# Optimization experiments

Hardware: AMD Instinct MI355X
Metric: run time of the kernel (lower is better)

## Reference

```python
import jax, jax.numpy as jnp
import numpy as np

N_COM = 100  # number of communities


def _gat(x, src, dst, ew, W, a_s, a_d):
    # Weighted multi-head GAT layer. x: [N,F], src/dst: [E], ew: [E]
    N = x.shape[0]
    H, dh = a_s.shape
    h = (x @ W).reshape(N, H, dh)              # [N,H,dh]
    hs, hd = h[src], h[dst]                     # [E,H,dh]
    e = jax.nn.leaky_relu((hs * a_s).sum(-1) + (hd * a_d).sum(-1), 0.2)  # [E,H]
    m = jax.ops.segment_max(e, dst, num_segments=N)  # [N,H] stable softmax max
    m = jnp.where(jnp.isfinite(m), m, 0.0)
    ex = jnp.exp(e - m[dst]) * ew[:, None]      # edge-weighted attention numerator
    den = jax.ops.segment_sum(ex, dst, num_segments=N)          # [N,H]
    num = jax.ops.segment_sum(ex[:, :, None] * hs, dst, num_segments=N)  # [N,H,dh]
    out = num / (den[:, :, None] + 1e-16)
    return jax.nn.elu(out.reshape(N, H * dh))


def _meso(x, part, D):
    # WeiPool_noW: degree-weighted mean pooling per community, scattered back to nodes
    num = jax.ops.segment_sum(D[:, None] * x, part, num_segments=N_COM)  # [C,d]
    den = jax.ops.segment_sum(D, part, num_segments=N_COM)               # [C]
    mean = num / (den[:, None] + 1e-16)
    return mean[part]                                                     # [N,d]


def _lstm_cell(h, c, x, Wx, Wh, b):
    z = x @ Wx + h @ Wh + b
    i, f, g, o = jnp.split(z, 4, axis=-1)
    c = jax.nn.sigmoid(f) * c + jax.nn.sigmoid(i) * jnp.tanh(g)
    h = jax.nn.sigmoid(o) * jnp.tanh(c)
    return h, c


def setup_inputs() -> dict:
    key = jax.random.key(0)
    ks = jax.random.split(key, 20)
    T, N, E, F = 8, 10000, 320000, 128
    H = 4
    d1, d2 = 128, 64            # micro_dims[1], micro_dims[2]
    d_rnn = 128                 # RNN_dims[1]; RNN input = 2*d2 = 128
    d_dec = 64                  # decoder_dims[1]
    s = 0.05
    inp = {
        'feat': jax.random.normal(ks[0], (T, N, F), jnp.float32),
        'edge_weight': jax.random.uniform(ks[1], (T, E), jnp.float32),
        'D': jax.random.uniform(ks[2], (T, N), jnp.float32),
        'W1': jax.random.normal(ks[3], (F, d1), jnp.float32) * s,
        'a_src1': jax.random.normal(ks[4], (H, d1 // H), jnp.float32) * s,
        'a_dst1': jax.random.normal(ks[5], (H, d1 // H), jnp.float32) * s,
        'W2': jax.random.normal(ks[6], (d1, d2), jnp.float32) * s,
        'a_src2': jax.random.normal(ks[7], (H, d2 // H), jnp.float32) * s,
        'a_dst2': jax.random.normal(ks[8], (H, d2 // H), jnp.float32) * s,
        'Wx': jax.random.normal(ks[9], (2 * d2, 4 * d_rnn), jnp.float32) * s,
        'Wh': jax.random.normal(ks[10], (d_rnn, 4 * d_rnn), jnp.float32) * s,
        'b_lstm': jnp.zeros((4 * d_rnn,), jnp.float32),
        'emb_W': jax.random.normal(ks[11], (d_rnn, d_dec), jnp.float32) * s,
        'emb_b': jnp.zeros((d_dec,), jnp.float32),
        'scal_W': jax.random.normal(ks[12], (d_rnn, d_dec), jnp.float32) * s,
        'scal_b': jnp.zeros((d_dec,), jnp.float32),
        'edge_index': jax.random.randint(ks[13], (T, 2, E), 0, N, jnp.int64),
        'partition': jax.random.randint(ks[14], (T, N), 0, N_COM, jnp.int64),
    }
    return inp


def reference(feat, edge_weight, D, W1, a_src1, a_dst1, W2, a_src2, a_dst2,
              Wx, Wh, b_lstm, emb_W, emb_b, scal_W, scal_b,
              edge_index, partition):
    T, N, _ = feat.shape
    src, dst = edge_index[:, 0], edge_index[:, 1]          # [T,E]
    gat = jax.vmap(_gat, in_axes=(0, 0, 0, 0, None, None, None))
    g1 = gat(feat, src, dst, edge_weight, W1, a_src1, a_dst1)   # [T,N,d1]
    g2 = gat(g1, src, dst, edge_weight, W2, a_src2, a_dst2)     # [T,N,d2]
    meso = jax.vmap(_meso)(g2, partition, D)                    # [T,N,d2]
    agg = jnp.concatenate([g2, meso], axis=-1)                  # [T,N,2*d2]

    d_h = Wh.shape[0]
    h0 = jnp.zeros((N, d_h), feat.dtype)

    def step(carry, x):
        h, c = carry
        h, c = _lstm_cell(h, c, x, Wx, Wh, b_lstm)
        return (h, c), h

    _, hs = jax.lax.scan(step, (h0, h0), agg)                   # [T,N,d_h]
    h_last = hs[-1]

    emb = jnp.tanh(h_last @ emb_W + emb_b)                      # decoder emb path
    emb = emb / jnp.linalg.norm(emb, axis=0, keepdims=True)     # F.normalize dim=0
    scal = jax.nn.sigmoid(h_last @ scal_W + scal_b)             # decoder scal path
    S = scal @ scal.T                                            # [N,N]
    G = emb @ emb.T
    sq = jnp.diag(G)
    dist = -(sq[:, None] + sq[None, :] - 2.0 * G)                # -||e_i - e_j||^2
    adj_est = 1.0 + jnp.tanh(dist * S)
    return adj_est
```

## Files before the change

kernel.cpp:

```cpp
#include <hip/hip_runtime.h>
#include <cstddef>
#include <cstdint>

#define T_   8
#define N_   10000
#define E_   320000
#define F_   128
#define D1_  128
#define D2_  64
#define DR_  128
#define NC_  100
#define TN_  (T_*N_)
#define TE_  (T_*E_)
#define NPAD_ 10112

typedef __attribute__((ext_vector_type(8))) short bf16x8;
typedef __attribute__((ext_vector_type(8))) ushort u16x8;
typedef __attribute__((ext_vector_type(4))) float f32x4;

__device__ __forceinline__ float bf2f(ushort u) {
    return __uint_as_float(((unsigned int)u) << 16);
}
__device__ __forceinline__ ushort f2bf(float f) {
    unsigned int u = __float_as_uint(f);
    unsigned int r = (u + 0x7FFFu + ((u >> 16) & 1u)) >> 16;
    return (ushort)r;
}
__device__ __forceinline__ float fast_tanh(float x) {
    float t = __expf(2.f * x);
    return 1.f - 2.f / (t + 1.f);
}
__device__ __forceinline__ float fast_sigmoid(float x) {
    return 1.f / (1.f + __expf(-x));
}

__global__ __launch_bounds__(256) void conv_feat(const float* __restrict__ src,
                                                 ushort* __restrict__ dst, int n8)
{
    int idx = blockIdx.x * 256 + threadIdx.x;
    if (idx >= n8) return;
    const float4* s = (const float4*)src + (size_t)idx * 2;
    float4 x = s[0], y = s[1];
    u16x8 o;
    o[0]=f2bf(x.x); o[1]=f2bf(x.y); o[2]=f2bf(x.z); o[3]=f2bf(x.w);
    o[4]=f2bf(y.x); o[5]=f2bf(y.y); o[6]=f2bf(y.z); o[7]=f2bf(y.w);
    *((u16x8*)dst + idx) = o;
}

__global__ __launch_bounds__(256) void conv_weights(
    const float* __restrict__ W1, const float* __restrict__ W2,
    const float* __restrict__ Wx, const float* __restrict__ Wh,
    const float* __restrict__ eW, const float* __restrict__ sW,
    ushort* __restrict__ W1T, ushort* __restrict__ W2T,
    ushort* __restrict__ WxT, ushort* __restrict__ WhT,
    ushort* __restrict__ eWT, ushort* __restrict__ sWT)
{
    int idx = blockIdx.x * 256 + threadIdx.x;
    if (idx < 16384)       { int n=idx>>7,   k=idx&127;            W1T[idx]=f2bf(W1[k*128+n]); }
    else if (idx < 24576)  { int l=idx-16384;  int n=l>>7,k=l&127; W2T[l]=f2bf(W2[k*64+n]); }
    else if (idx < 90112)  { int l=idx-24576;  int n=l>>7,k=l&127; WxT[l]=f2bf(Wx[k*512+n]); }
    else if (idx < 155648) { int l=idx-90112;  int n=l>>7,k=l&127; WhT[l]=f2bf(Wh[k*512+n]); }
    else if (idx < 163840) { int l=idx-155648; int n=l>>7,k=l&127; eWT[l]=f2bf(eW[k*64+n]); }
    else if (idx < 172032) { int l=idx-163840; int n=l>>7,k=l&127; sWT[l]=f2bf(sW[k*64+n]); }
}

__global__ __launch_bounds__(256) void gemm_bf16(
    const ushort* __restrict__ A, const ushort* __restrict__ BT,
    float* __restrict__ Cf, ushort* __restrict__ Cb,
    const float* __restrict__ bias, const float* __restrict__ addsrc,
    int M, int K, int Nc, int act)
{
    int w = threadIdx.x >> 6, lane = threadIdx.x & 63;
    int quad = lane >> 4, l16 = lane & 15;
    int m0 = blockIdx.y * 128 + w * 32;
    int n0 = blockIdx.x * 64;
    f32x4 zf = {0.f, 0.f, 0.f, 0.f};
    f32x4 acc[2][4];
    #pragma unroll
    for (int rt = 0; rt < 2; ++rt)
        #pragma unroll
        for (int ct = 0; ct < 4; ++ct) acc[rt][ct] = zf;

    for (int k0 = 0; k0 < K; k0 += 32) {
        int kk = k0 + quad * 8;
        bf16x8 a0 = *(const bf16x8*)(A + (size_t)(m0 + l16) * K + kk);
        bf16x8 a1 = *(const bf16x8*)(A + (size_t)(m0 + 16 + l16) * K + kk);
        bf16x8 b[4];
        #pragma unroll
        for (int ct = 0; ct < 4; ++ct)
            b[ct] = *(const bf16x8*)(BT + (size_t)(n0 + ct * 16 + l16) * K + kk);
        #pragma unroll
        for (int ct = 0; ct < 4; ++ct) {
            acc[0][ct] = __builtin_amdgcn_mfma_f32_16x16x32_bf16(a0, b[ct], acc[0][ct], 0, 0, 0);
            acc[1][ct] = __builtin_amdgcn_mfma_f32_16x16x32_bf16(a1, b[ct], acc[1][ct], 0, 0, 0);
        }
    }

    #pragma unroll
    for (int rt = 0; rt < 2; ++rt) {
        int ibase = m0 + rt * 16 + quad * 4;
        #pragma unroll
        for (int r = 0; r < 4; ++r) {
            int i = ibase + r;
            if (i >= M) continue;
            #pragma unroll
            for (int ct = 0; ct < 4; ++ct) {
                int j = n0 + ct * 16 + l16;
                float v = acc[rt][ct][r];
                if (bias)   v += bias[j];
                if (addsrc) v += addsrc[(size_t)i * Nc + j];
                if (act == 1)      v = fast_tanh(v);
                else if (act == 2) v = fast_sigmoid(v);
                if (Cf) Cf[(size_t)i * Nc + j] = v;
                if (Cb) Cb[(size_t)i * Nc + j] = f2bf(v);
            }
        }
    }
}

__global__ __launch_bounds__(256) void att_vec128(
    const ushort* __restrict__ h, const float* __restrict__ a_src,
    const float* __restrict__ a_dst, float* __restrict__ as_out,
    float* __restrict__ ad_out, int rows)
{
    int wid  = (blockIdx.x * 256 + threadIdx.x) >> 6;
    int lane = threadIdx.x & 63;
    if (wid >= rows) return;
    const ushort* hr = h + (size_t)wid * 128;
    float v0 = bf2f(hr[lane]), v1 = bf2f(hr[64 + lane]);
    float pa0 = v0 * a_src[lane], pa1 = v1 * a_src[64 + lane];
    float pd0 = v0 * a_dst[lane], pd1 = v1 * a_dst[64 + lane];
    #pragma unroll
    for (int m = 1; m <= 16; m <<= 1) {
        pa0 += __shfl_xor(pa0, m); pa1 += __shfl_xor(pa1, m);
        pd0 += __shfl_xor(pd0, m); pd1 += __shfl_xor(pd1, m);
    }
    if ((lane & 31) == 0) {
        int g = lane >> 5;
        as_out[wid * 4 + g] = pa0; as_out[wid * 4 + 2 + g] = pa1;
        ad_out[wid * 4 + g] = pd0; ad_out[wid * 4 + 2 + g] = pd1;
    }
}

__global__ __launch_bounds__(256) void att_vec64(
    const ushort* __restrict__ h, const float* __restrict__ a_src,
    const float* __restrict__ a_dst, float* __restrict__ as_out,
    float* __restrict__ ad_out, int rows)
{
    int wid  = (blockIdx.x * 256 + threadIdx.x) >> 6;
    int lane = threadIdx.x & 63;
    if (wid >= rows) return;
    float v = bf2f(h[(size_t)wid * 64 + lane]);
    float pa = v * a_src[lane], pd = v * a_dst[lane];
    #pragma unroll
    for (int m = 1; m <= 8; m <<= 1) { pa += __shfl_xor(pa, m); pd += __shfl_xor(pd, m); }
    if ((lane & 15) == 0) {
        int g = lane >> 4;
        as_out[wid * 4 + g] = pa; ad_out[wid * 4 + g] = pd;
    }
}

__global__ void count_edges(const int* __restrict__ eidx, int* __restrict__ counts)
{
    int idx = blockIdx.x * 256 + threadIdx.x;
    if (idx >= TE_) return;
    int t = idx / E_, e = idx - t * E_;
    int d = eidx[(size_t)t * 2 * E_ + E_ + e];
    atomicAdd(&counts[t * N_ + d], 1);
}

__global__ __launch_bounds__(1024) void scan_per_t(
    const int* __restrict__ counts, int* __restrict__ rowptr, int* __restrict__ cursor)
{
    const int CH = 10;
    int t = blockIdx.x, i = threadIdx.x;
    int base0 = t * N_;
    int cnt[CH];
    int s = 0;
    int g0 = i * CH;
    #pragma unroll
    for (int q = 0; q < CH; ++q) {
        int g = g0 + q;
        cnt[q] = (g < N_) ? counts[base0 + g] : 0;
        s += cnt[q];
    }
    __shared__ int buf[1024];
    buf[i] = s;
    __syncthreads();
    for (int off = 1; off < 1024; off <<= 1) {
        int v = (i >= off) ? buf[i - off] : 0;
        __syncthreads();
        buf[i] += v;
        __syncthreads();
    }
    int run = t * E_ + buf[i] - s;
    #pragma unroll
    for (int q = 0; q < CH; ++q) {
        int g = g0 + q;
        if (g < N_) {
            rowptr[base0 + g] = run;
            cursor[base0 + g] = run;
            run += cnt[q];
        }
    }
    if (t == T_ - 1 && i == 1023) rowptr[T_ * N_] = TE_;
}

__global__ void fill_csr(const int* __restrict__ eidx, const float* __restrict__ ew,
                         int* __restrict__ cursor, int* __restrict__ src_csr,
                         float* __restrict__ ew_csr)
{
    int idx = blockIdx.x * 256 + threadIdx.x;
    if (idx >= TE_) return;
    int t = idx / E_, e = idx - t * E_;
    int s = eidx[(size_t)t * 2 * E_ + e];
    int d = eidx[(size_t)t * 2 * E_ + E_ + e];
    float w = ew[(size_t)t * E_ + e];
    int pos = atomicAdd(&cursor[t * N_ + d], 1);
    src_csr[pos] = t * N_ + s;
    ew_csr[pos] = w;
}

__global__ __launch_bounds__(256) void gat_node_128(
    const ushort* __restrict__ h, const float* __restrict__ as,
    const float* __restrict__ ad, const int* __restrict__ rowptr,
    const int* __restrict__ src_csr, const float* __restrict__ ew_csr,
    ushort* __restrict__ outp, int rows)
{
    int wid  = (blockIdx.x * 256 + threadIdx.x) >> 6;
    int lane = threadIdx.x & 63;
    if (wid >= rows) return;
    int start = rowptr[wid], end = rowptr[wid + 1];
    int h0 = lane >> 5;
    float ad0 = ad[wid * 4 + h0], ad1 = ad[wid * 4 + 2 + h0];
    float acc0 = 0.f, acc1 = 0.f, den0 = 0.f, den1 = 0.f;

    int p = start;
    for (; p + 4 <= end; p += 4) {
        int s0 = src_csr[p+0], s1 = src_csr[p+1], s2 = src_csr[p+2], s3 = src_csr[p+3];
        float w0 = ew_csr[p+0], w1 = ew_csr[p+1], w2 = ew_csr[p+2], w3 = ew_csr[p+3];
        float4 A0 = *(const float4*)(as + (size_t)s0 * 4);
        float4 A1 = *(const float4*)(as + (size_t)s1 * 4);
        float4 A2 = *(const float4*)(as + (size_t)s2 * 4);
        float4 A3 = *(const float4*)(as + (size_t)s3 * 4);
        const ushort* q0 = h + (size_t)s0 * 128;
        const ushort* q1 = h + (size_t)s1 * 128;
        const ushort* q2 = h + (size_t)s2 * 128;
        const ushort* q3 = h + (size_t)s3 * 128;
        float hx0 = bf2f(q0[lane]), hy0 = bf2f(q0[64 + lane]);
        float hx1 = bf2f(q1[lane]), hy1 = bf2f(q1[64 + lane]);
        float hx2 = bf2f(q2[lane]), hy2 = bf2f(q2[64 + lane]);
        float hx3 = bf2f(q3[lane]), hy3 = bf2f(q3[64 + lane]);
        #define GSTEP(AA, ww, hx, hy) { \
            float e0 = (h0 ? AA.y : AA.x) + ad0; e0 = e0 > 0.f ? e0 : 0.2f * e0; \
            float e1 = (h0 ? AA.w : AA.z) + ad1; e1 = e1 > 0.f ? e1 : 0.2f * e1; \
            float x0 = __expf(e0) * ww, x1 = __expf(e1) * ww; \
            den0 += x0; den1 += x1; acc0 += x0 * hx; acc1 += x1 * hy; }
        GSTEP(A0, w0, hx0, hy0)
        GSTEP(A1, w1, hx1, hy1)
        GSTEP(A2, w2, hx2, hy2)
        GSTEP(A3, w3, hx3, hy3)
    }
    for (; p < end; ++p) {
        int s = src_csr[p];
        float w = ew_csr[p];
        float4 A = *(const float4*)(as + (size_t)s * 4);
        const ushort* q = h + (size_t)s * 128;
        float hx = bf2f(q[lane]), hy = bf2f(q[64 + lane]);
        GSTEP(A, w, hx, hy)
    }
    #undef GSTEP

    float o0 = acc0 / (den0 + 1e-16f);
    float o1 = acc1 / (den1 + 1e-16f);
    o0 = o0 > 0.f ? o0 : (__expf(o0) - 1.f);
    o1 = o1 > 0.f ? o1 : (__expf(o1) - 1.f);
    outp[(size_t)wid * 128 + lane]      = f2bf(o0);
    outp[(size_t)wid * 128 + 64 + lane] = f2bf(o1);
}

__global__ __launch_bounds__(256) void gat_node_64(
    const ushort* __restrict__ h, const float* __restrict__ as,
    const float* __restrict__ ad, const int* __restrict__ rowptr,
    const int* __restrict__ src_csr, const float* __restrict__ ew_csr,
    ushort* __restrict__ outp, int rows)
{
    int wid  = (blockIdx.x * 256 + threadIdx.x) >> 6;
    int lane = threadIdx.x & 63;
    if (wid >= rows) return;
    int start = rowptr[wid], end = rowptr[wid + 1];
    int hh = lane >> 4;
    float adv = ad[wid * 4 + hh];
    float acc = 0.f, den = 0.f;

    int p = start;
    for (; p + 4 <= end; p += 4) {
        int s0 = src_csr[p+0], s1 = src_csr[p+1], s2 = src_csr[p+2], s3 = src_csr[p+3];
        float w0 = ew_csr[p+0], w1 = ew_csr[p+1], w2 = ew_csr[p+2], w3 = ew_csr[p+3];
        float4 A0 = *(const float4*)(as + (size_t)s0 * 4);
        float4 A1 = *(const float4*)(as + (size_t)s1 * 4);
        float4 A2 = *(const float4*)(as + (size_t)s2 * 4);
        float4 A3 = *(const float4*)(as + (size_t)s3 * 4);
        float hv0 = bf2f(h[(size_t)s0 * 64 + lane]);
        float hv1 = bf2f(h[(size_t)s1 * 64 + lane]);
        float hv2 = bf2f(h[(size_t)s2 * 64 + lane]);
        float hv3 = bf2f(h[(size_t)s3 * 64 + lane]);
        #define GSTEP64(AA, ww, hv) { \
            float e = (hh & 2 ? (hh & 1 ? AA.w : AA.z) : (hh & 1 ? AA.y : AA.x)) + adv; \
            e = e > 0.f ? e : 0.2f * e; \
            float x = __expf(e) * ww; \
            den += x; acc += x * hv; }
        GSTEP64(A0, w0, hv0)
        GSTEP64(A1, w1, hv1)
        GSTEP64(A2, w2, hv2)
        GSTEP64(A3, w3, hv3)
    }
    for (; p < end; ++p) {
        int s = src_csr[p];
        float w = ew_csr[p];
        float4 A = *(const float4*)(as + (size_t)s * 4);
        float hv = bf2f(h[(size_t)s * 64 + lane]);
        GSTEP64(A, w, hv)
    }
    #undef GSTEP64

    float o = acc / (den + 1e-16f);
    o = o > 0.f ? o : (__expf(o) - 1.f);
    outp[(size_t)wid * 64 + lane] = f2bf(o);
}

__global__ __launch_bounds__(256) void meso_acc(
    const ushort* __restrict__ g2, const int* __restrict__ part,
    const float* __restrict__ Dw, float* __restrict__ msum, float* __restrict__ mden)
{
    int wid  = (blockIdx.x * 256 + threadIdx.x) >> 6;
    int lane = threadIdx.x & 63;
    if (wid >= TN_) return;
    int t = wid / N_;
    int p = part[wid];
    float dv = Dw[wid];
    atomicAdd(&msum[((size_t)(t * NC_ + p) << 6) + lane], dv * bf2f(g2[(size_t)wid * 64 + lane]));
    if (lane == 0) atomicAdd(&mden[t * NC_ + p], dv);
}

__global__ void agg_assemble(
    const ushort* __restrict__ g2, const int* __restrict__ part,
    const float* __restrict__ msum, const float* __restrict__ mden,
    ushort* __restrict__ agg)
{
    int idx = blockIdx.x * 256 + threadIdx.x;
    int row = idx >> 7, d = idx & 127;
    ushort v;
    if (d < 64) {
        v = g2[(size_t)row * 64 + d];
    } else {
        int t = row / N_;
        int p = part[row];
        v = f2bf(msum[((size_t)(t * NC_ + p) << 6) + (d - 64)] / (mden[t * NC_ + p] + 1e-16f));
    }
    agg[idx] = v;
}

__global__ __launch_bounds__(512) void lstm_fused(
    const ushort* __restrict__ hin, const ushort* __restrict__ WhT,
    const float* __restrict__ zx, float* __restrict__ c,
    ushort* __restrict__ hout)
{
    __shared__ float zt[32][516];
    int w = threadIdx.x >> 6, lane = threadIdx.x & 63;
    int quad = lane >> 4, l16 = lane & 15;
    int m0 = blockIdx.x * 32;
    int n0 = w * 64;

    f32x4 zf = {0.f, 0.f, 0.f, 0.f};
    f32x4 acc[2][4];
    #pragma unroll
    for (int rt = 0; rt < 2; ++rt)
        #pragma unroll
        for (int ct = 0; ct < 4; ++ct) acc[rt][ct] = zf;

    #pragma unroll
    for (int k0 = 0; k0 < 128; k0 += 32) {
        int kk = k0 + quad * 8;
        bf16x8 a0 = *(const bf16x8*)(hin + (size_t)(m0 + l16) * 128 + kk);
        bf16x8 a1 = *(const bf16x8*)(hin + (size_t)(m0 + 16 + l16) * 128 + kk);
        bf16x8 b[4];
        #pragma unroll
        for (int ct = 0; ct < 4; ++ct)
            b[ct] = *(const bf16x8*)(WhT + (size_t)(n0 + ct * 16 + l16) * 128 + kk);
        #pragma unroll
        for (int ct = 0; ct < 4; ++ct) {
            acc[0][ct] = __builtin_amdgcn_mfma_f32_16x16x32_bf16(a0, b[ct], acc[0][ct], 0, 0, 0);
            acc[1][ct] = __builtin_amdgcn_mfma_f32_16x16x32_bf16(a1, b[ct], acc[1][ct], 0, 0, 0);
        }
    }

    #pragma unroll
    for (int rt = 0; rt < 2; ++rt) {
        #pragma unroll
        for (int r = 0; r < 4; ++r) {
            int li = rt * 16 + quad * 4 + r;
            size_t gi = (size_t)(m0 + li);
            #pragma unroll
            for (int ct = 0; ct < 4; ++ct) {
                int j = n0 + ct * 16 + l16;
                zt[li][j] = acc[rt][ct][r] + zx[gi * 512 + j];
            }
        }
    }
    __syncthreads();

    int r  = threadIdx.x >> 4;
    int j0 = (threadIdx.x & 15) * 8;
    int gi = m0 + r;
    if (gi < N_) {
        f32x4 vi[2], vf[2], vg[2], vo[2], vc[2];
        #pragma unroll
        for (int hb = 0; hb < 2; ++hb) {
            int jj = j0 + hb * 4;
            vi[hb] = *(const f32x4*)&zt[r][jj];
            vf[hb] = *(const f32x4*)&zt[r][128 + jj];
            vg[hb] = *(const f32x4*)&zt[r][256 + jj];
            vo[hb] = *(const f32x4*)&zt[r][384 + jj];
            vc[hb] = *(const f32x4*)(c + (size_t)gi * 128 + jj);
        }
        u16x8 ho;
        #pragma unroll
        for (int e = 0; e < 8; ++e) {
            int hb = e >> 2, q = e & 3;
            float si = fast_sigmoid(vi[hb][q]);
            float sf = fast_sigmoid(vf[hb][q]);
            float so = fast_sigmoid(vo[hb][q]);
            float cn = sf * vc[hb][q] + si * fast_tanh(vg[hb][q]);
            vc[hb][q] = cn;
            ho[e] = f2bf(so * fast_tanh(cn));
        }
        *(f32x4*)(c + (size_t)gi * 128 + j0)     = vc[0];
        *(f32x4*)(c + (size_t)gi * 128 + j0 + 4) = vc[1];
        *(u16x8*)(hout + (size_t)gi * 128 + j0)  = ho;
    }
}

__global__ __launch_bounds__(256) void col_sumsq(const float* __restrict__ emb,
                                                 float* __restrict__ colss)
{
    int tid = threadIdx.x;
    int col = tid & 63, rq = tid >> 6;
    float s = 0.f;
    for (int r = blockIdx.x * 4 + rq; r < N_; r += 40 * 4) {
        float v = emb[(size_t)r * 64 + col];
        s += v * v;
    }
    __shared__ float red[256];
    red[tid] = s;
    __syncthreads();
    if (tid < 64)
        atomicAdd(&colss[tid], red[tid] + red[tid + 64] + red[tid + 128] + red[tid + 192]);
}

__global__ __launch_bounds__(256) void norm_rows(const float* __restrict__ emb,
                                                 const float* __restrict__ colss,
                                                 ushort* __restrict__ embb,
                                                 float* __restrict__ sq, int rows)
{
    int wid  = (blockIdx.x * 256 + threadIdx.x) >> 6;
    int lane = threadIdx.x & 63;
    if (wid >= rows) return;
    float nv = emb[(size_t)wid * 64 + lane] / sqrtf(colss[lane]);
    ushort ub = f2bf(nv);
    embb[(size_t)wid * 64 + lane] = ub;
    float nq = bf2f(ub);
    float q = nq * nq;
    #pragma unroll
    for (int m = 1; m <= 32; m <<= 1) q += __shfl_xor(q, m);
    if (lane == 0) sq[wid] = q;
}

#define FTJ_   5
#define FCOLS_ (FTJ_*128)

__global__ __launch_bounds__(256) void final_adj_mfma(
    const ushort* __restrict__ embb, const ushort* __restrict__ scalb,
    const float* __restrict__ sq, float* __restrict__ outp)
{
    __shared__ float cur[128][132];
    __shared__ float edg[2][64][16];

    int w = threadIdx.x >> 6, lane = threadIdx.x & 63;
    int quad = lane >> 4, l16 = lane & 15;
    int bi = blockIdx.y * 128;
    int Wb = blockIdx.x * FCOLS_;
    int wi = bi + (w >> 1) * 64;

    float sqi[4];
    #pragma unroll
    for (int rt = 0; rt < 4; ++rt) sqi[rt] = sq[wi + rt * 16 + l16];

    int tLast = (N_ - 1 - Wb) / 128;
    if (tLast > FTJ_ - 1) tLast = FTJ_ - 1;

    for (int t = 0; t <= tLast; ++t) {
        int Wt = Wb + t * 128;
        int wj = Wt + (w & 1) * 64;

        f32x4 zf = {0.f, 0.f, 0.f, 0.f};
        f32x4 accG[4][4], accS[4][4];
        #pragma unroll
        for (int rt = 0; rt < 4; ++rt)
            #pragma unroll
            for (int ct = 0; ct < 4; ++ct) { accG[rt][ct] = zf; accS[rt][ct] = zf; }

        #pragma unroll
        for (int ks = 0; ks < 2; ++ks) {
            int k0 = ks * 32 + quad * 8;
            bf16x8 ae[4], af[4], be[4], bs[4];
            #pragma unroll
            for (int q = 0; q < 4; ++q) {
                int ri = wi + q * 16 + l16;
                int rj = wj + q * 16 + l16;
                ae[q] = *(const bf16x8*)(embb  + (size_t)ri * 64 + k0);
                af[q] = *(const bf16x8*)(scalb + (size_t)ri * 64 + k0);
                be[q] = *(const bf16x8*)(embb  + (size_t)rj * 64 + k0);
                bs[q] = *(const bf16x8*)(scalb + (size_t)rj * 64 + k0);
            }
            #pragma unroll
            for (int rt = 0; rt < 4; ++rt)
                #pragma unroll
                for (int ct = 0; ct < 4; ++ct) {
                    accG[rt][ct] = __builtin_amdgcn_mfma_f32_16x16x32_bf16(be[ct], ae[rt], accG[rt][ct], 0, 0, 0);
                    accS[rt][ct] = __builtin_amdgcn_mfma_f32_16x16x32_bf16(bs[ct], af[rt], accS[rt][ct], 0, 0, 0);
                }
        }

        __syncthreads();

        #pragma unroll
        for (int rt = 0; rt < 4; ++rt) {
            int li = (w >> 1) * 64 + rt * 16 + l16;
            float si = sqi[rt];
            #pragma unroll
            for (int ct = 0; ct < 4; ++ct) {
                int lj = (w & 1) * 64 + ct * 16 + quad * 4;
                const float4 sj = *(const float4*)(sq + Wt + lj);
                float sjr[4] = { sj.x, sj.y, sj.z, sj.w };
                f32x4 v;
                #pragma unroll
                for (int r = 0; r < 4; ++r) {
                    float G = accG[rt][ct][r], S = accS[rt][ct][r];
                    float dist = 2.f * G - si - sjr[r];
                    float e = __expf(2.f * dist * S);
                    v[r] = 2.f - 2.f / (e + 1.f);
                }
                *(f32x4*)&cur[li][lj] = v;
                if ((w & 1) && ct == 3 && (li & 1))
                    *(f32x4*)&edg[t & 1][li >> 1][quad * 4] = v;
            }
        }

        __syncthreads();

        int lane5 = lane & 31;
        #pragma unroll
        for (int pass = 0; pass < 16; ++pass) {
            int r = pass * 8 + (lane >> 5) * 4 + w;
            int i = bi + r;
            if (i < N_) {
                if (!(r & 1)) {
                    int gcol = Wt + lane5 * 4;
                    if (gcol < N_)
                        __builtin_nontemporal_store(*(const f32x4*)&cur[r][lane5 * 4],
                            (f32x4*)(outp + (size_t)i * N_ + gcol));
                } else {
                    int gcol = Wt - 16 + lane5 * 4;
                    if ((t > 0 || lane5 >= 4) && gcol >= 0 && gcol < N_) {
                        f32x4 v;
                        if (lane5 < 4) v = *(const f32x4*)&edg[(t & 1) ^ 1][r >> 1][lane5 * 4];
                        else           v = *(const f32x4*)&cur[r][lane5 * 4 - 16];
                        __builtin_nontemporal_store(v,
                            (f32x4*)(outp + (size_t)i * N_ + gcol));
                    }
                }
            }
        }
    }

    {
        int tid = threadIdx.x;
        int r = ((tid >> 2) << 1) | 1;
        int k = (tid & 3) * 4;
        int i = bi + r;
        int gcol = Wb + tLast * 128 + 112 + k;
        if (i < N_ && gcol < N_) {
            f32x4 v = *(const f32x4*)&cur[r][112 + k];
            __builtin_nontemporal_store(v, (f32x4*)(outp + (size_t)i * N_ + gcol));
        }
    }
}

extern "C" void kernel_launch(void* const* d_in, const int* in_sizes, int n_in,
                              void* d_out, int out_size, void* d_ws, size_t ws_size,
                              hipStream_t stream)
{
    (void)in_sizes; (void)n_in; (void)out_size; (void)ws_size;
    const float* feat    = (const float*)d_in[0];
    const float* eweight = (const float*)d_in[1];
    const float* Dw      = (const float*)d_in[2];
    const float* W1      = (const float*)d_in[3];
    const float* a_src1  = (const float*)d_in[4];
    const float* a_dst1  = (const float*)d_in[5];
    const float* W2      = (const float*)d_in[6];
    const float* a_src2  = (const float*)d_in[7];
    const float* a_dst2  = (const float*)d_in[8];
    const float* Wx      = (const float*)d_in[9];
    const float* Wh      = (const float*)d_in[10];
    const float* b_lstm  = (const float*)d_in[11];
    const float* emb_W   = (const float*)d_in[12];
    const float* emb_b   = (const float*)d_in[13];
    const float* scal_W  = (const float*)d_in[14];
    const float* scal_b  = (const float*)d_in[15];
    const int*   eidx    = (const int*)d_in[16];
    const int*   part    = (const int*)d_in[17];

    float* out = (float*)d_out;
    ushort* h1b   = (ushort*)(out + 0);
    ushort* g1b   = (ushort*)(out + 5120000);
    ushort* h2b   = (ushort*)(out + 10240000);
    ushort* g2b   = (ushort*)(out + 12800000);
    float* as1    = out + 15360000;
    float* ad1    = out + 15680000;
    float* as2    = out + 16000000;
    float* ad2    = out + 16320000;
    int*   rowptr = (int*)(out + 16640000);
    int*   cursor = (int*)(out + 16720064);
    int*   counts = (int*)(out + 16800064);
    int*   src_csr= (int*)(out + 16880064);
    float* ew_csr = out + 19440064;
    float* msum   = out + 22000064;
    float* mden   = out + 22051264;
    ushort* aggb  = (ushort*)(out + 22052064);
    float* ZX     = out + 27172064;
    float* cstate = out + 73252064;
    ushort* hbf   = (ushort*)(out + 74532064);
    ushort* featb = (ushort*)(out + 75179232);
    ushort* W1T   = (ushort*)(out + 80299232);
    ushort* W2T   = (ushort*)(out + 80307424);
    ushort* WxT   = (ushort*)(out + 80311520);
    ushort* WhT   = (ushort*)(out + 80344288);
    ushort* eWT   = (ushort*)(out + 80377056);
    ushort* sWT   = (ushort*)(out + 80381152);
    float* embf   = out + 80385248;
    float* colss  = out + 81025248;

    ushort* embb  = (ushort*)d_ws;
    ushort* scalb = embb + (size_t)NPAD_ * 64;
    float*  sq    = (float*)(scalb + (size_t)NPAD_ * 64);

    hipMemsetAsync(counts, 0, TN_ * sizeof(int), stream);
    hipMemsetAsync(msum, 0, (T_ * NC_ * 64 + T_ * NC_) * sizeof(float), stream);
    hipMemsetAsync(cstate, 0, (size_t)N_ * DR_ * sizeof(float), stream);
    hipMemsetAsync(hbf, 0, (size_t)NPAD_ * DR_ * sizeof(ushort), stream);
    hipMemsetAsync(colss, 0, 64 * sizeof(float), stream);

    conv_feat<<<5000, 256, 0, stream>>>(feat, featb, TN_ * F_ / 8);
    conv_weights<<<672, 256, 0, stream>>>(W1, W2, Wx, Wh, emb_W, scal_W,
                                          W1T, W2T, WxT, WhT, eWT, sWT);

    gemm_bf16<<<dim3(2, 625), 256, 0, stream>>>(featb, W1T, nullptr, h1b, nullptr, nullptr, TN_, 128, 128, 0);
    att_vec128<<<TN_/4, 256, 0, stream>>>(h1b, a_src1, a_dst1, as1, ad1, TN_);
    count_edges<<<(TE_+255)/256, 256, 0, stream>>>(eidx, counts);
    scan_per_t<<<T_, 1024, 0, stream>>>(counts, rowptr, cursor);
    fill_csr<<<(TE_+255)/256, 256, 0, stream>>>(eidx, eweight, cursor, src_csr, ew_csr);
    gat_node_128<<<TN_/4, 256, 0, stream>>>(h1b, as1, ad1, rowptr, src_csr, ew_csr, g1b, TN_);

    gemm_bf16<<<dim3(1, 625), 256, 0, stream>>>(g1b, W2T, nullptr, h2b, nullptr, nullptr, TN_, 128, 64, 0);
    att_vec64<<<TN_/4, 256, 0, stream>>>(h2b, a_src2, a_dst2, as2, ad2, TN_);
    gat_node_64<<<TN_/4, 256, 0, stream>>>(h2b, as2, ad2, rowptr, src_csr, ew_csr, g2b, TN_);

    meso_acc<<<TN_/4, 256, 0, stream>>>(g2b, part, Dw, msum, mden);
    agg_assemble<<<TN_*128/256, 256, 0, stream>>>(g2b, part, msum, mden, aggb);

    gemm_bf16<<<dim3(8, 625), 256, 0, stream>>>(aggb, WxT, ZX, nullptr, b_lstm, nullptr, TN_, 128, 512, 0);
    for (int t = 0; t < T_; ++t)
        lstm_fused<<<(N_ + 31) / 32, 512, 0, stream>>>(hbf, WhT, ZX + (size_t)t * N_ * 512,
                                                       cstate, hbf);

    gemm_bf16<<<dim3(1, 79), 256, 0, stream>>>(hbf, eWT, embf, nullptr, emb_b, nullptr, N_, 128, 64, 1);
    gemm_bf16<<<dim3(1, 79), 256, 0, stream>>>(hbf, sWT, nullptr, scalb, scal_b, nullptr, N_, 128, 64, 2);
    col_sumsq<<<40, 256, 0, stream>>>(embf, colss);
    norm_rows<<<(N_+3)/4, 256, 0, stream>>>(embf, colss, embb, sq, N_);

    final_adj_mfma<<<dim3(16, 79), 256, 0, stream>>>(embb, scalb, sq, out);
}
```

Before: 1.640 ms.

## Interleave CSR src/weight, widen GAT edge unroll, privatize meso pooling in LDS

Stores each CSR edge as an interleaved int2 (source index, weight bits) so the GAT aggregation kernels fetch both with one 16-byte vector load per two edges. The inner loop unrolls to 8 edges after an alignment peel, putting more independent gathers in flight. Meso pooling switches from per-node global atomics to per-block LDS histograms per timestep that are flushed once with global atomics, cutting global atomic contention. The cost is more register pressure from the wider unroll and only 128 blocks for the meso kernel.

```diff
diff --git a/kernel.cpp b/kernel.cpp
--- a/kernel.cpp
+++ b/kernel.cpp
@@ -207,8 +207,7 @@
 }
 
 __global__ void fill_csr(const int* __restrict__ eidx, const float* __restrict__ ew,
-                         int* __restrict__ cursor, int* __restrict__ src_csr,
-                         float* __restrict__ ew_csr)
+                         int* __restrict__ cursor, int2* __restrict__ csr)
 {
     int idx = blockIdx.x * 256 + threadIdx.x;
     if (idx >= TE_) return;
@@ -217,15 +216,13 @@
     int d = eidx[(size_t)t * 2 * E_ + E_ + e];
     float w = ew[(size_t)t * E_ + e];
     int pos = atomicAdd(&cursor[t * N_ + d], 1);
-    src_csr[pos] = t * N_ + s;
-    ew_csr[pos] = w;
+    csr[pos] = make_int2(t * N_ + s, __float_as_int(w));
 }
 
 __global__ __launch_bounds__(256) void gat_node_128(
     const ushort* __restrict__ h, const float* __restrict__ as,
     const float* __restrict__ ad, const int* __restrict__ rowptr,
-    const int* __restrict__ src_csr, const float* __restrict__ ew_csr,
-    ushort* __restrict__ outp, int rows)
+    const int2* __restrict__ csr, ushort* __restrict__ outp, int rows)
 {
     int wid  = (blockIdx.x * 256 + threadIdx.x) >> 6;
     int lane = threadIdx.x & 63;
@@ -235,38 +232,50 @@
     float ad0 = ad[wid * 4 + h0], ad1 = ad[wid * 4 + 2 + h0];
     float acc0 = 0.f, acc1 = 0.f, den0 = 0.f, den1 = 0.f;
 
+    #define GSTEP(AA, ww, hx, hy) { \
+        float e0 = (h0 ? AA.y : AA.x) + ad0; e0 = e0 > 0.f ? e0 : 0.2f * e0; \
+        float e1 = (h0 ? AA.w : AA.z) + ad1; e1 = e1 > 0.f ? e1 : 0.2f * e1; \
+        float x0 = __expf(e0) * ww, x1 = __expf(e1) * ww; \
+        den0 += x0; den1 += x1; acc0 += x0 * hx; acc1 += x1 * hy; }
+
     int p = start;
-    for (; p + 4 <= end; p += 4) {
-        int s0 = src_csr[p+0], s1 = src_csr[p+1], s2 = src_csr[p+2], s3 = src_csr[p+3];
-        float w0 = ew_csr[p+0], w1 = ew_csr[p+1], w2 = ew_csr[p+2], w3 = ew_csr[p+3];
-        float4 A0 = *(const float4*)(as + (size_t)s0 * 4);
-        float4 A1 = *(const float4*)(as + (size_t)s1 * 4);
-        float4 A2 = *(const float4*)(as + (size_t)s2 * 4);
-        float4 A3 = *(const float4*)(as + (size_t)s3 * 4);
-        const ushort* q0 = h + (size_t)s0 * 128;
-        const ushort* q1 = h + (size_t)s1 * 128;
-        const ushort* q2 = h + (size_t)s2 * 128;
-        const ushort* q3 = h + (size_t)s3 * 128;
-        float hx0 = bf2f(q0[lane]), hy0 = bf2f(q0[64 + lane]);
-        float hx1 = bf2f(q1[lane]), hy1 = bf2f(q1[64 + lane]);
-        float hx2 = bf2f(q2[lane]), hy2 = bf2f(q2[64 + lane]);
-        float hx3 = bf2f(q3[lane]), hy3 = bf2f(q3[64 + lane]);
-        #define GSTEP(AA, ww, hx, hy) { \
-            float e0 = (h0 ? AA.y : AA.x) + ad0; e0 = e0 > 0.f ? e0 : 0.2f * e0; \
-            float e1 = (h0 ? AA.w : AA.z) + ad1; e1 = e1 > 0.f ? e1 : 0.2f * e1; \
-            float x0 = __expf(e0) * ww, x1 = __expf(e1) * ww; \
-            den0 += x0; den1 += x1; acc0 += x0 * hx; acc1 += x1 * hy; }
-        GSTEP(A0, w0, hx0, hy0)
-        GSTEP(A1, w1, hx1, hy1)
-        GSTEP(A2, w2, hx2, hy2)
-        GSTEP(A3, w3, hx3, hy3)
+    if ((p & 1) && p < end) {
+        int2 E = csr[p];
+        float4 A = *(const float4*)(as + (size_t)E.x * 4);
+        const ushort* q = h + (size_t)E.x * 128;
+        float hx = bf2f(q[lane]), hy = bf2f(q[64 + lane]);
+        float w = __int_as_float(E.y);
+        GSTEP(A, w, hx, hy)
+        ++p;
+    }
+    for (; p + 8 <= end; p += 8) {
+        int4 e0 = *(const int4*)(csr + p);
+        int4 e1 = *(const int4*)(csr + p + 2);
+        int4 e2 = *(const int4*)(csr + p + 4);
+        int4 e3 = *(const int4*)(csr + p + 6);
+        int ss[8] = { e0.x, e0.z, e1.x, e1.z, e2.x, e2.z, e3.x, e3.z };
+        float wwv[8] = { __int_as_float(e0.y), __int_as_float(e0.w),
+                         __int_as_float(e1.y), __int_as_float(e1.w),
+                         __int_as_float(e2.y), __int_as_float(e2.w),
+                         __int_as_float(e3.y), __int_as_float(e3.w) };
+        float4 Av[8];
+        #pragma unroll
+        for (int q = 0; q < 8; ++q) Av[q] = *(const float4*)(as + (size_t)ss[q] * 4);
+        float hx[8], hy[8];
+        #pragma unroll
+        for (int q = 0; q < 8; ++q) {
+            const ushort* hp = h + (size_t)ss[q] * 128;
+            hx[q] = bf2f(hp[lane]); hy[q] = bf2f(hp[64 + lane]);
+        }
+        #pragma unroll
+        for (int q = 0; q < 8; ++q) GSTEP(Av[q], wwv[q], hx[q], hy[q])
     }
     for (; p < end; ++p) {
-        int s = src_csr[p];
-        float w = ew_csr[p];
-        float4 A = *(const float4*)(as + (size_t)s * 4);
-        const ushort* q = h + (size_t)s * 128;
+        int2 E = csr[p];
+        float4 A = *(const float4*)(as + (size_t)E.x * 4);
+        const ushort* q = h + (size_t)E.x * 128;
         float hx = bf2f(q[lane]), hy = bf2f(q[64 + lane]);
+        float w = __int_as_float(E.y);
         GSTEP(A, w, hx, hy)
     }
     #undef GSTEP
@@ -282,8 +291,7 @@
 __global__ __launch_bounds__(256) void gat_node_64(
     const ushort* __restrict__ h, const float* __restrict__ as,
     const float* __restrict__ ad, const int* __restrict__ rowptr,
-    const int* __restrict__ src_csr, const float* __restrict__ ew_csr,
-    ushort* __restrict__ outp, int rows)
+    const int2* __restrict__ csr, ushort* __restrict__ outp, int rows)
 {
     int wid  = (blockIdx.x * 256 + threadIdx.x) >> 6;
     int lane = threadIdx.x & 63;
@@ -293,33 +301,45 @@
     float adv = ad[wid * 4 + hh];
     float acc = 0.f, den = 0.f;
 
+    #define GSTEP64(AA, ww, hv) { \
+        float e = (hh & 2 ? (hh & 1 ? AA.w : AA.z) : (hh & 1 ? AA.y : AA.x)) + adv; \
+        e = e > 0.f ? e : 0.2f * e; \
+        float x = __expf(e) * ww; \
+        den += x; acc += x * hv; }
+
     int p = start;
-    for (; p + 4 <= end; p += 4) {
-        int s0 = src_csr[p+0], s1 = src_csr[p+1], s2 = src_csr[p+2], s3 = src_csr[p+3];
-        float w0 = ew_csr[p+0], w1 = ew_csr[p+1], w2 = ew_csr[p+2], w3 = ew_csr[p+3];
-        float4 A0 = *(const float4*)(as + (size_t)s0 * 4);
-        float4 A1 = *(const float4*)(as + (size_t)s1 * 4);
-        float4 A2 = *(const float4*)(as + (size_t)s2 * 4);
-        float4 A3 = *(const float4*)(as + (size_t)s3 * 4);
-        float hv0 = bf2f(h[(size_t)s0 * 64 + lane]);
-        float hv1 = bf2f(h[(size_t)s1 * 64 + lane]);
-        float hv2 = bf2f(h[(size_t)s2 * 64 + lane]);
-        float hv3 = bf2f(h[(size_t)s3 * 64 + lane]);
-        #define GSTEP64(AA, ww, hv) { \
-            float e = (hh & 2 ? (hh & 1 ? AA.w : AA.z) : (hh & 1 ? AA.y : AA.x)) + adv; \
-            e = e > 0.f ? e : 0.2f * e; \
-            float x = __expf(e) * ww; \
-            den += x; acc += x * hv; }
-        GSTEP64(A0, w0, hv0)
-        GSTEP64(A1, w1, hv1)
-        GSTEP64(A2, w2, hv2)
-        GSTEP64(A3, w3, hv3)
+    if ((p & 1) && p < end) {
+        int2 E = csr[p];
+        float4 A = *(const float4*)(as + (size_t)E.x * 4);
+        float hv = bf2f(h[(size_t)E.x * 64 + lane]);
+        float w = __int_as_float(E.y);
+        GSTEP64(A, w, hv)
+        ++p;
+    }
+    for (; p + 8 <= end; p += 8) {
+        int4 e0 = *(const int4*)(csr + p);
+        int4 e1 = *(const int4*)(csr + p + 2);
+        int4 e2 = *(const int4*)(csr + p + 4);
+        int4 e3 = *(const int4*)(csr + p + 6);
+        int ss[8] = { e0.x, e0.z, e1.x, e1.z, e2.x, e2.z, e3.x, e3.z };
+        float wwv[8] = { __int_as_float(e0.y), __int_as_float(e0.w),
+                         __int_as_float(e1.y), __int_as_float(e1.w),
+                         __int_as_float(e2.y), __int_as_float(e2.w),
+                         __int_as_float(e3.y), __int_as_float(e3.w) };
+        float4 Av[8];
+        #pragma unroll
+        for (int q = 0; q < 8; ++q) Av[q] = *(const float4*)(as + (size_t)ss[q] * 4);
+        float hv[8];
+        #pragma unroll
+        for (int q = 0; q < 8; ++q) hv[q] = bf2f(h[(size_t)ss[q] * 64 + lane]);
+        #pragma unroll
+        for (int q = 0; q < 8; ++q) GSTEP64(Av[q], wwv[q], hv[q])
     }
     for (; p < end; ++p) {
-        int s = src_csr[p];
-        float w = ew_csr[p];
-        float4 A = *(const float4*)(as + (size_t)s * 4);
-        float hv = bf2f(h[(size_t)s * 64 + lane]);
+        int2 E = csr[p];
+        float4 A = *(const float4*)(as + (size_t)E.x * 4);
+        float hv = bf2f(h[(size_t)E.x * 64 + lane]);
+        float w = __int_as_float(E.y);
         GSTEP64(A, w, hv)
     }
     #undef GSTEP64
@@ -329,18 +349,35 @@
     outp[(size_t)wid * 64 + lane] = f2bf(o);
 }
 
-__global__ __launch_bounds__(256) void meso_acc(
+__global__ __launch_bounds__(256) void meso_lds(
     const ushort* __restrict__ g2, const int* __restrict__ part,
     const float* __restrict__ Dw, float* __restrict__ msum, float* __restrict__ mden)
 {
-    int wid  = (blockIdx.x * 256 + threadIdx.x) >> 6;
-    int lane = threadIdx.x & 63;
-    if (wid >= TN_) return;
-    int t = wid / N_;
-    int p = part[wid];
-    float dv = Dw[wid];
-    atomicAdd(&msum[((size_t)(t * NC_ + p) << 6) + lane], dv * bf2f(g2[(size_t)wid * 64 + lane]));
-    if (lane == 0) atomicAdd(&mden[t * NC_ + p], dv);
+    __shared__ float hist[NC_][64];
+    __shared__ float hden[NC_];
+    int t   = blockIdx.x >> 4;
+    int blk = blockIdx.x & 15;
+    int tid = threadIdx.x;
+    for (int i = tid; i < NC_ * 64; i += 256) ((float*)hist)[i] = 0.f;
+    for (int i = tid; i < NC_; i += 256) hden[i] = 0.f;
+    __syncthreads();
+
+    int wv = tid >> 6, lane = tid & 63;
+    int wl = blk * 4 + wv;
+    for (int n = wl; n < N_; n += 64) {
+        int gid = t * N_ + n;
+        int pc = part[gid];
+        float dv = Dw[gid];
+        float val = dv * bf2f(g2[(size_t)gid * 64 + lane]);
+        atomicAdd(&hist[pc][lane], val);
+        if (lane == 0) atomicAdd(&hden[pc], dv);
+    }
+    __syncthreads();
+
+    for (int i = tid; i < NC_ * 64; i += 256)
+        atomicAdd(&msum[(size_t)t * NC_ * 64 + i], ((float*)hist)[i]);
+    for (int i = tid; i < NC_; i += 256)
+        atomicAdd(&mden[t * NC_ + i], hden[i]);
 }
 
 __global__ void agg_assemble(
@@ -633,8 +670,7 @@
     int*   rowptr = (int*)(out + 16640000);
     int*   cursor = (int*)(out + 16720064);
     int*   counts = (int*)(out + 16800064);
-    int*   src_csr= (int*)(out + 16880064);
-    float* ew_csr = out + 19440064;
+    int2*  csr_sw = (int2*)(out + 16880064);
     float* msum   = out + 22000064;
     float* mden   = out + 22051264;
     ushort* aggb  = (ushort*)(out + 22052064);
@@ -669,14 +705,14 @@
     att_vec128<<<TN_/4, 256, 0, stream>>>(h1b, a_src1, a_dst1, as1, ad1, TN_);
     count_edges<<<(TE_+255)/256, 256, 0, stream>>>(eidx, counts);
     scan_per_t<<<T_, 1024, 0, stream>>>(counts, rowptr, cursor);
-    fill_csr<<<(TE_+255)/256, 256, 0, stream>>>(eidx, eweight, cursor, src_csr, ew_csr);
-    gat_node_128<<<TN_/4, 256, 0, stream>>>(h1b, as1, ad1, rowptr, src_csr, ew_csr, g1b, TN_);
+    fill_csr<<<(TE_+255)/256, 256, 0, stream>>>(eidx, eweight, cursor, csr_sw);
+    gat_node_128<<<TN_/4, 256, 0, stream>>>(h1b, as1, ad1, rowptr, csr_sw, g1b, TN_);
 
     gemm_bf16<<<dim3(1, 625), 256, 0, stream>>>(g1b, W2T, nullptr, h2b, nullptr, nullptr, TN_, 128, 64, 0);
     att_vec64<<<TN_/4, 256, 0, stream>>>(h2b, a_src2, a_dst2, as2, ad2, TN_);
-    gat_node_64<<<TN_/4, 256, 0, stream>>>(h2b, as2, ad2, rowptr, src_csr, ew_csr, g2b, TN_);
-
-    meso_acc<<<TN_/4, 256, 0, stream>>>(g2b, part, Dw, msum, mden);
+    gat_node_64<<<TN_/4, 256, 0, stream>>>(h2b, as2, ad2, rowptr, csr_sw, g2b, TN_);
+
+    meso_lds<<<T_ * 16, 256, 0, stream>>>(g2b, part, Dw, msum, mden);
     agg_assemble<<<TN_*128/256, 256, 0, stream>>>(g2b, part, msum, mden, aggb);
 
     gemm_bf16<<<dim3(8, 625), 256, 0, stream>>>(aggb, WxT, ZX, nullptr, b_lstm, nullptr, TN_, 128, 512, 0);
```

Result: no change. 1.608 ms (-1.9%).
